# Kernel tuning notes

Hardware: AMD Instinct MI355X
Metric: run time of the kernel (lower is better)

Reference implementation:

```python
import jax, jax.numpy as jnp
import numpy as np

LN_EPS = 1e-5        # torch default LayerNorm eps
DEB_EPS = 1e-7       # deberta-v3 layer_norm_eps
ATT_SPAN = 256       # deberta-v3-base position_buckets -> pos_ebd_size
MAX_REL = 100        # config.max_relative_positions override


def _ln(x, g, b, eps):
    m = x.mean(-1, keepdims=True)
    v = jnp.var(x, axis=-1, keepdims=True)
    return (x - m) * jax.lax.rsqrt(v + eps) * g + b


def _lin(x, w, b):
    return x @ w.T + b


def _rel_buckets(L):
    # build_relative_position + make_log_bucket_position (bucket_size=256, max_position=100)
    rel = jnp.arange(L, dtype=jnp.int32)[:, None] - jnp.arange(L, dtype=jnp.int32)[None, :]
    mid = ATT_SPAN // 2
    sign = jnp.sign(rel)
    abs_pos = jnp.where((rel < mid) & (rel > -mid), mid - 1, jnp.abs(rel))
    log_pos = jnp.ceil(jnp.log(abs_pos.astype(jnp.float32) / mid)
                       / np.float32(np.log((MAX_REL - 1) / mid)) * (mid - 1)) + mid
    return jnp.where(abs_pos <= mid, rel, (log_pos * sign).astype(jnp.int32))


def _forward(ints, floats):
    type_ids, landmark_ids, mask = ints
    (xs, ys, zs, type_emb, landmark_emb, type_ln_g, type_ln_b, lm_ln_g, lm_ln_b,
     pos_w, pos_b, lt_in_w, lt_in_b, lt_out_w, lt_out_b, lt_ln1_g, lt_ln1_b,
     lt_ff1_w, lt_ff1_b, lt_ff2_w, lt_ff2_b, lt_ln2_g, lt_ln2_b,
     rel_emb, rel_ln_g, rel_ln_b, dq_w, dq_b, dk_w, dk_b, dv_w, dv_b,
     dao_w, dao_b, da_ln_g, da_ln_b, di_w, di_b, do_w, do_b, do_ln_g, do_ln_b,
     head_w, head_b) = floats

    # embeddings (padding_idx=0 -> zero row & zero grad) + layernorms + pos projection
    te = _ln(type_emb[type_ids] * (type_ids != 0)[..., None].astype(jnp.float32), type_ln_g, type_ln_b, LN_EPS)
    le = _ln(landmark_emb[landmark_ids] * (landmark_ids != 0)[..., None].astype(jnp.float32), lm_ln_g, lm_ln_b, LN_EPS)
    pe = _lin(jnp.stack([xs, ys, zs], -1), pos_w, pos_b)
    fts = jnp.concatenate([te, le, pe], -1)                  # [B,F,L,768]
    B, F, L, D = fts.shape
    h = fts.reshape(B * F, L, D)

    # --- nn.TransformerEncoderLayer over landmarks (post-norm, relu, nhead=1) ---
    q, k, v = jnp.split(_lin(h, lt_in_w, lt_in_b), 3, axis=-1)
    probs = jax.nn.softmax(jnp.einsum('bqd,bkd->bqk', q, k) / np.float32(np.sqrt(D)), axis=-1)
    attn = _lin(jnp.einsum('bqk,bkd->bqd', probs, v), lt_out_w, lt_out_b)
    h = _ln(h + attn, lt_ln1_g, lt_ln1_b, LN_EPS)
    ff = _lin(jax.nn.relu(_lin(h, lt_ff1_w, lt_ff1_b)), lt_ff2_w, lt_ff2_b)
    h = _ln(h + ff, lt_ln2_g, lt_ln2_b, LN_EPS)

    h = h.reshape(B, F, L, D).mean(2)                        # [B,F,768]

    # --- DebertaV2 layer over frames (disentangled attention, 1 head) ---
    m = mask[:, :, 0] > 0                                    # [B,F]
    q = _lin(h, dq_w, dq_b)
    k = _lin(h, dk_w, dk_b)
    v = _lin(h, dv_w, dv_b)
    scale = np.float32(np.sqrt(D * 3))                       # scale_factor = 1 + len({c2p,p2c})
    scores = jnp.einsum('bqd,bkd->bqk', q, k) / scale
    rel_ln = _ln(rel_emb, rel_ln_g, rel_ln_b, DEB_EPS)       # norm_rel_ebd='layer_norm'
    pos_q = _lin(rel_ln, dq_w, dq_b)                         # share_att_key=True
    pos_k = _lin(rel_ln, dk_w, dk_b)
    rel = _rel_buckets(F)                                    # [F,F]
    c2p_idx = jnp.clip(rel + ATT_SPAN, 0, 2 * ATT_SPAN - 1)
    c2p = jnp.einsum('bqd,rd->bqr', q, pos_k)                # [B,F,512]
    c2p = jnp.take_along_axis(c2p, jnp.broadcast_to(c2p_idx[None], (B, F, F)), axis=-1)
    p2c_idx = jnp.clip(-rel + ATT_SPAN, 0, 2 * ATT_SPAN - 1)
    p2c = jnp.einsum('bkd,rd->bkr', k, pos_q)                # [B,F,512]
    p2c = jnp.take_along_axis(p2c, jnp.broadcast_to(p2c_idx[None], (B, F, F)), axis=-1)
    scores = scores + (c2p + jnp.swapaxes(p2c, -1, -2)) / scale
    amask = m[:, :, None] & m[:, None, :]                    # XSoftmax mask
    probs = jax.nn.softmax(jnp.where(amask, scores, jnp.finfo(scores.dtype).min), axis=-1)
    probs = jnp.where(amask, probs, 0.0)
    ctx = jnp.einsum('bqk,bkd->bqd', probs, v)
    h = _ln(_lin(ctx, dao_w, dao_b) + h, da_ln_g, da_ln_b, DEB_EPS)
    inter = jax.nn.gelu(_lin(h, di_w, di_b), approximate=False)
    h = _ln(_lin(inter, do_w, do_b) + h, do_ln_g, do_ln_b, DEB_EPS)

    return _lin(h.mean(1), head_w, head_b)                   # [B,250]


def setup_inputs():
    ks = iter(jax.random.split(jax.random.key(0), 64))
    B, F, L, E, D, DF, NC = 8, 80, 100, 256, 768, 3072, 250
    def w(*shape):
        return jax.random.normal(next(ks), shape, dtype=jnp.float32) * 0.02
    z = lambda *s: jnp.zeros(s, jnp.float32)
    o = lambda *s: jnp.ones(s, jnp.float32)
    return {
        "type_ids": jax.random.randint(next(ks), (B, F, L), 0, 12, dtype=jnp.int32),
        "landmark_ids": jax.random.randint(next(ks), (B, F, L), 0, 127, dtype=jnp.int32),
        "xs": jax.random.normal(next(ks), (B, F, L), dtype=jnp.float32),
        "ys": jax.random.normal(next(ks), (B, F, L), dtype=jnp.float32),
        "zs": jax.random.normal(next(ks), (B, F, L), dtype=jnp.float32),
        "mask": jnp.ones((B, F, L), jnp.int32),
        "type_emb": w(12, E), "landmark_emb": w(127, E),
        "type_ln_g": o(E), "type_ln_b": z(E), "lm_ln_g": o(E), "lm_ln_b": z(E),
        "pos_w": w(E, 3), "pos_b": z(E),
        "lt_in_w": w(3 * D, D), "lt_in_b": z(3 * D), "lt_out_w": w(D, D), "lt_out_b": z(D),
        "lt_ln1_g": o(D), "lt_ln1_b": z(D),
        "lt_ff1_w": w(D, D), "lt_ff1_b": z(D), "lt_ff2_w": w(D, D), "lt_ff2_b": z(D),
        "lt_ln2_g": o(D), "lt_ln2_b": z(D),
        "rel_emb": w(2 * ATT_SPAN, D), "rel_ln_g": o(D), "rel_ln_b": z(D),
        "dq_w": w(D, D), "dq_b": z(D), "dk_w": w(D, D), "dk_b": z(D), "dv_w": w(D, D), "dv_b": z(D),
        "dao_w": w(D, D), "dao_b": z(D), "da_ln_g": o(D), "da_ln_b": z(D),
        "di_w": w(DF, D), "di_b": z(DF), "do_w": w(D, DF), "do_b": z(D),
        "do_ln_g": o(D), "do_ln_b": z(D),
        "head_w": w(NC, D), "head_b": z(NC),
    }


def reference(type_ids, landmark_ids, xs, ys, zs, mask, type_emb, landmark_emb,
              type_ln_g, type_ln_b, lm_ln_g, lm_ln_b, pos_w, pos_b,
              lt_in_w, lt_in_b, lt_out_w, lt_out_b, lt_ln1_g, lt_ln1_b,
              lt_ff1_w, lt_ff1_b, lt_ff2_w, lt_ff2_b, lt_ln2_g, lt_ln2_b,
              rel_emb, rel_ln_g, rel_ln_b, dq_w, dq_b, dk_w, dk_b, dv_w, dv_b,
              dao_w, dao_b, da_ln_g, da_ln_b, di_w, di_b, do_w, do_b,
              do_ln_g, do_ln_b, head_w, head_b):
    floats = (xs, ys, zs, type_emb, landmark_emb, type_ln_g, type_ln_b, lm_ln_g, lm_ln_b,
              pos_w, pos_b, lt_in_w, lt_in_b, lt_out_w, lt_out_b, lt_ln1_g, lt_ln1_b,
              lt_ff1_w, lt_ff1_b, lt_ff2_w, lt_ff2_b, lt_ln2_g, lt_ln2_b,
              rel_emb, rel_ln_g, rel_ln_b, dq_w, dq_b, dk_w, dk_b, dv_w, dv_b,
              dao_w, dao_b, da_ln_g, da_ln_b, di_w, di_b, do_w, do_b, do_ln_g, do_ln_b,
              head_w, head_b)
    return _forward((type_ids, landmark_ids, mask), floats)
```

## Files before the change

### kernel.cpp

```cpp
#include <hip/hip_runtime.h>

using short8v = __attribute__((ext_vector_type(8))) short;
using float4v = __attribute__((ext_vector_type(4))) float;

__device__ __forceinline__ unsigned short f2bf(float f) {
  unsigned int u = __float_as_uint(f);
  u += 0x7FFF + ((u >> 16) & 1);
  return (unsigned short)(u >> 16);
}
__device__ __forceinline__ float bf2f(unsigned short u) {
  return __uint_as_float((unsigned int)u << 16);
}

__device__ __forceinline__ int swz(int row, int c) {
  return row * 64 + (c ^ ((row & 7) << 3));
}

template<int BM, int ACT, bool OUTBF, int RES>
__global__ __launch_bounds__(256) void gemm_mfma(
    const unsigned short* __restrict__ A, const unsigned short* __restrict__ B,
    const float* __restrict__ bias, const void* __restrict__ resid, int ldr,
    void* __restrict__ Cv,
    int M, int N, int K, int lda, int ldb, int ldc,
    long long sA, long long sB, long long sC, long long sBias, float alpha)
{
  constexpr int NF = BM / 32;
  A += (long long)blockIdx.z * sA;
  B += (long long)blockIdx.z * sB;
  if (bias) bias += (long long)blockIdx.z * sBias;
  const int m0 = blockIdx.y * BM, n0 = blockIdx.x * BM;

  __shared__ __align__(16) unsigned short As[BM * 64];
  __shared__ __align__(16) unsigned short Bs[BM * 64];

  const int tid = threadIdx.x;
  const int w = tid >> 6, lane = tid & 63;
  const int wr = w >> 1, wc = w & 1;

  const int r0 = tid >> 3;
  const int c8 = (tid & 7) * 8;
  int ra[NF], rb[NF], soff[NF];
  #pragma unroll
  for (int i = 0; i < NF; ++i) {
    int r = m0 + r0 + i * 32; ra[i] = r < M - 1 ? r : M - 1;
    int q = n0 + r0 + i * 32; rb[i] = q < N - 1 ? q : N - 1;
    soff[i] = swz(r0 + i * 32, c8);
  }

  const int fr = lane & 15;
  const int fk = (lane >> 4) * 8;

  float4v acc[NF][NF] = {};

  short8v pa[NF], pb[NF];
  #pragma unroll
  for (int i = 0; i < NF; ++i) {
    pa[i] = *(const short8v*)(A + (long long)ra[i] * lda + c8);
    pb[i] = *(const short8v*)(B + (long long)rb[i] * ldb + c8);
  }

  for (int k0 = 0; k0 < K; k0 += 64) {
    __syncthreads();
    #pragma unroll
    for (int i = 0; i < NF; ++i) {
      *(short8v*)&As[soff[i]] = pa[i];
      *(short8v*)&Bs[soff[i]] = pb[i];
    }
    __syncthreads();
    if (k0 + 64 < K) {
      #pragma unroll
      for (int i = 0; i < NF; ++i) {
        pa[i] = *(const short8v*)(A + (long long)ra[i] * lda + k0 + 64 + c8);
        pb[i] = *(const short8v*)(B + (long long)rb[i] * ldb + k0 + 64 + c8);
      }
    }
    #pragma unroll
    for (int kk = 0; kk < 2; ++kk) {
      short8v a[NF], b[NF];
      #pragma unroll
      for (int i = 0; i < NF; ++i) {
        a[i] = *(const short8v*)&As[swz(wr * (NF * 16) + i * 16 + fr, kk * 32 + fk)];
        b[i] = *(const short8v*)&Bs[swz(wc * (NF * 16) + i * 16 + fr, kk * 32 + fk)];
      }
      #pragma unroll
      for (int mi = 0; mi < NF; ++mi)
        #pragma unroll
        for (int ni = 0; ni < NF; ++ni)
          acc[mi][ni] = __builtin_amdgcn_mfma_f32_16x16x32_bf16(a[mi], b[ni], acc[mi][ni], 0, 0, 0);
    }
  }

  const int ccol0 = n0 + wc * (NF * 16) + (lane & 15);
  const int crow0 = m0 + wr * (NF * 16) + (lane >> 4) * 4;
  float* Cf = (float*)Cv + (long long)blockIdx.z * sC;
  unsigned short* Cb = (unsigned short*)Cv + (long long)blockIdx.z * sC;
  #pragma unroll
  for (int ni = 0; ni < NF; ++ni) {
    const int col = ccol0 + ni * 16;
    if (col >= N) continue;
    const float bs = bias ? bias[col] : 0.f;
    #pragma unroll
    for (int mi = 0; mi < NF; ++mi) {
      #pragma unroll
      for (int r = 0; r < 4; ++r) {
        const int row = crow0 + mi * 16 + r;
        if (row >= M) continue;
        float v = acc[mi][ni][r] * alpha + bs;
        if (RES == 1) v += bf2f(((const unsigned short*)resid)[(long long)row * ldr + col]);
        if (RES == 2) v += ((const float*)resid)[(long long)row * ldr + col];
        if (ACT == 1) v = fmaxf(v, 0.f);
        if (ACT == 2) v = 0.5f * v * (1.f + erff(v * 0.70710678118654752f));
        if (OUTBF) Cb[(long long)row * ldc + col] = f2bf(v);
        else       Cf[(long long)row * ldc + col] = v;
      }
    }
  }
}

static void mg(hipStream_t st, int bm, int act, bool outbf, int res,
               const unsigned short* A, const unsigned short* B,
               const float* bias, const void* resid, int ldr, void* C,
               int M, int N, int K, int lda, int ldb, int ldc,
               long long sA, long long sB, long long sC, long long sBias,
               int bat, float alpha)
{
  dim3 grid((N + bm - 1) / bm, (M + bm - 1) / bm, bat);
  dim3 blk(256);
  #define GEMM_CALL(BM_, A_, O_, R_) \
    gemm_mfma<BM_, A_, O_, R_><<<grid, blk, 0, st>>>(A, B, bias, resid, ldr, C, \
        M, N, K, lda, ldb, ldc, sA, sB, sC, sBias, alpha)
  if (bm == 128) {
    if (outbf) {
      if (act == 1)       GEMM_CALL(128, 1, true, 0);
      else if (res == 1)  GEMM_CALL(128, 0, true, 1);
      else                GEMM_CALL(128, 0, true, 0);
    } else {
      GEMM_CALL(128, 0, false, 0);
    }
  } else {
    if (outbf) {
      if (act == 2)       GEMM_CALL(64, 2, true, 0);
      else                GEMM_CALL(64, 0, true, 0);
    } else {
      if (res == 2)       GEMM_CALL(64, 0, false, 2);
      else                GEMM_CALL(64, 0, false, 0);
    }
  }
  #undef GEMM_CALL
}

struct ConvArgs {
  const float* s[10];
  unsigned short* d[10];
  long long off[11];
};
__global__ __launch_bounds__(256) void convall_kernel(ConvArgs a, long long tot)
{
  const long long i = ((long long)blockIdx.x * 256 + threadIdx.x) * 4;
  if (i >= tot) return;
  int t = 0;
  while (i >= a.off[t + 1]) ++t;
  const long long j = i - a.off[t];
  const float4 v = *(const float4*)(a.s[t] + j);
  const unsigned int lo = (unsigned int)f2bf(v.x) | ((unsigned int)f2bf(v.y) << 16);
  const unsigned int hi = (unsigned int)f2bf(v.z) | ((unsigned int)f2bf(v.w) << 16);
  *(uint2*)(a.d[t] + j) = make_uint2(lo, hi);
}

__global__ __launch_bounds__(256) void embed_kernel(
    const int* __restrict__ tids, const int* __restrict__ lids,
    const float* __restrict__ xs, const float* __restrict__ ys, const float* __restrict__ zs,
    const float* __restrict__ temb, const float* __restrict__ lemb,
    const float* __restrict__ tg, const float* __restrict__ tb,
    const float* __restrict__ lg, const float* __restrict__ lb,
    const float* __restrict__ pw, const float* __restrict__ pb,
    unsigned short* __restrict__ hb)
{
  const int tok = blockIdx.x * 4 + (threadIdx.x >> 6);
  const int lane = threadIdx.x & 63;
  const int e0 = lane * 4;
  const int ti = tids[tok], li = lids[tok];
  float4 tv = make_float4(0.f, 0.f, 0.f, 0.f);
  float4 lv = make_float4(0.f, 0.f, 0.f, 0.f);
  if (ti != 0) tv = *(const float4*)(temb + ti * 256 + e0);
  if (li != 0) lv = *(const float4*)(lemb + li * 256 + e0);

  float s0 = tv.x + tv.y + tv.z + tv.w;
  float s1 = tv.x * tv.x + tv.y * tv.y + tv.z * tv.z + tv.w * tv.w;
  float s2 = lv.x + lv.y + lv.z + lv.w;
  float s3 = lv.x * lv.x + lv.y * lv.y + lv.z * lv.z + lv.w * lv.w;
  #pragma unroll
  for (int off = 32; off > 0; off >>= 1) {
    s0 += __shfl_xor(s0, off, 64);
    s1 += __shfl_xor(s1, off, 64);
    s2 += __shfl_xor(s2, off, 64);
    s3 += __shfl_xor(s3, off, 64);
  }
  const float mt = s0 * (1.f / 256.f), vt = s1 * (1.f / 256.f) - mt * mt;
  const float ml = s2 * (1.f / 256.f), vl = s3 * (1.f / 256.f) - ml * ml;
  const float rt = rsqrtf(vt + 1e-5f), rl = rsqrtf(vl + 1e-5f);

  const float4 tg4 = *(const float4*)(tg + e0), tb4 = *(const float4*)(tb + e0);
  const float4 lg4 = *(const float4*)(lg + e0), lb4 = *(const float4*)(lb + e0);
  const size_t base = (size_t)tok * 768;
  ushort4 o;
  o.x = f2bf((tv.x - mt) * rt * tg4.x + tb4.x);
  o.y = f2bf((tv.y - mt) * rt * tg4.y + tb4.y);
  o.z = f2bf((tv.z - mt) * rt * tg4.z + tb4.z);
  o.w = f2bf((tv.w - mt) * rt * tg4.w + tb4.w);
  *(ushort4*)(hb + base + e0) = o;
  o.x = f2bf((lv.x - ml) * rl * lg4.x + lb4.x);
  o.y = f2bf((lv.y - ml) * rl * lg4.y + lb4.y);
  o.z = f2bf((lv.z - ml) * rl * lg4.z + lb4.z);
  o.w = f2bf((lv.w - ml) * rl * lg4.w + lb4.w);
  *(ushort4*)(hb + base + 256 + e0) = o;

  const float X = xs[tok], Y = ys[tok], Z = zs[tok];
  const float4 w0 = *(const float4*)(pw + 12 * lane);
  const float4 w1 = *(const float4*)(pw + 12 * lane + 4);
  const float4 w2 = *(const float4*)(pw + 12 * lane + 8);
  const float4 pb4 = *(const float4*)(pb + e0);
  o.x = f2bf(w0.x * X + w0.y * Y + w0.z * Z + pb4.x);
  o.y = f2bf(w0.w * X + w1.x * Y + w1.y * Z + pb4.y);
  o.z = f2bf(w1.z * X + w1.w * Y + w2.x * Z + pb4.z);
  o.w = f2bf(w2.y * X + w2.z * Y + w2.w * Z + pb4.w);
  *(ushort4*)(hb + base + 512 + e0) = o;
}

template<int XBF, int RBF>
__global__ __launch_bounds__(256) void ln_kernel(
    const void* __restrict__ x, const void* __restrict__ res,
    const float* __restrict__ g, const float* __restrict__ b,
    float* __restrict__ yf, unsigned short* __restrict__ yb,
    int nrows, float eps)
{
  const int row = blockIdx.x * 4 + (threadIdx.x >> 6);
  if (row >= nrows) return;
  const int lane = threadIdx.x & 63;
  const size_t base = (size_t)row * 768;
  const int e0 = lane * 12;
  float v[12];
  #pragma unroll
  for (int j = 0; j < 3; ++j) {
    if (XBF) {
      const ushort4 u = *(const ushort4*)((const unsigned short*)x + base + e0 + 4 * j);
      v[4*j+0] = bf2f(u.x); v[4*j+1] = bf2f(u.y); v[4*j+2] = bf2f(u.z); v[4*j+3] = bf2f(u.w);
    } else {
      const float4 f = *(const float4*)((const float*)x + base + e0 + 4 * j);
      v[4*j+0] = f.x; v[4*j+1] = f.y; v[4*j+2] = f.z; v[4*j+3] = f.w;
    }
  }
  if (res) {
    #pragma unroll
    for (int j = 0; j < 3; ++j) {
      if (RBF) {
        const ushort4 u = *(const ushort4*)((const unsigned short*)res + base + e0 + 4 * j);
        v[4*j+0] += bf2f(u.x); v[4*j+1] += bf2f(u.y); v[4*j+2] += bf2f(u.z); v[4*j+3] += bf2f(u.w);
      } else {
        const float4 f = *(const float4*)((const float*)res + base + e0 + 4 * j);
        v[4*j+0] += f.x; v[4*j+1] += f.y; v[4*j+2] += f.z; v[4*j+3] += f.w;
      }
    }
  }
  float s = 0.f, ss = 0.f;
  #pragma unroll
  for (int j = 0; j < 12; ++j) { s += v[j]; ss += v[j] * v[j]; }
  #pragma unroll
  for (int off = 32; off > 0; off >>= 1) {
    s += __shfl_xor(s, off, 64);
    ss += __shfl_xor(ss, off, 64);
  }
  const float mean = s * (1.f / 768.f);
  const float rstd = rsqrtf(ss * (1.f / 768.f) - mean * mean + eps);
  #pragma unroll
  for (int j = 0; j < 3; ++j) {
    const float4 g4 = *(const float4*)(g + e0 + 4 * j);
    const float4 b4 = *(const float4*)(b + e0 + 4 * j);
    float o0 = (v[4*j+0] - mean) * rstd * g4.x + b4.x;
    float o1 = (v[4*j+1] - mean) * rstd * g4.y + b4.y;
    float o2 = (v[4*j+2] - mean) * rstd * g4.z + b4.z;
    float o3 = (v[4*j+3] - mean) * rstd * g4.w + b4.w;
    if (yf) *(float4*)(yf + base + e0 + 4 * j) = make_float4(o0, o1, o2, o3);
    if (yb) {
      ushort4 u; u.x = f2bf(o0); u.y = f2bf(o1); u.z = f2bf(o2); u.w = f2bf(o3);
      *(ushort4*)(yb + base + e0 + 4 * j) = u;
    }
  }
}

__global__ __launch_bounds__(256) void vtrans_kernel(
    const unsigned short* __restrict__ v, unsigned short* __restrict__ vt,
    int Lk, int rs, long long sIn, long long sOut)
{
  __shared__ unsigned short s[64][132];
  const int b = blockIdx.y, d0 = blockIdx.x * 64;
  const unsigned short* vb = v + (long long)b * sIn;
  unsigned short* ob = vt + (long long)b * sOut;
  for (int idx = threadIdx.x; idx < 128 * 64; idx += 256) {
    const int k = idx >> 6, dd = idx & 63;
    s[dd][k] = (k < Lk) ? vb[(long long)k * rs + d0 + dd] : (unsigned short)0;
  }
  __syncthreads();
  for (int idx = threadIdx.x; idx < 64 * 128; idx += 256) {
    const int dd = idx >> 7, k = idx & 127;
    ob[(long long)(d0 + dd) * 128 + k] = s[dd][k];
  }
}

__global__ __launch_bounds__(256) void sm2_kernel(
    const float* __restrict__ P32, unsigned short* __restrict__ Pbf, int nrows)
{
  const int rid = blockIdx.x * 4 + (threadIdx.x >> 6);
  if (rid >= nrows) return;
  const int z = rid / 100, q = rid - z * 100;
  const int lane = threadIdx.x & 63;
  const float* row = P32 + (size_t)z * 16384 + (size_t)q * 128;
  unsigned short* orow = Pbf + (size_t)z * 16384 + (size_t)q * 128;
  const float v0 = row[lane];
  const float v1 = (lane + 64 < 100) ? row[lane + 64] : -3.4e38f;
  float m = fmaxf(v0, v1);
  #pragma unroll
  for (int off = 32; off > 0; off >>= 1) m = fmaxf(m, __shfl_xor(m, off, 64));
  const float e0 = expf(v0 - m);
  const float e1 = (lane + 64 < 100) ? expf(v1 - m) : 0.f;
  float s = e0 + e1;
  #pragma unroll
  for (int off = 32; off > 0; off >>= 1) s += __shfl_xor(s, off, 64);
  const float inv = 1.f / s;
  orow[lane] = f2bf(e0 * inv);
  orow[lane + 64] = (lane + 64 < 100) ? f2bf(e1 * inv) : (unsigned short)0;
}

__global__ __launch_bounds__(256) void deb3_kernel(
    const float* __restrict__ sc,
    const float* __restrict__ c2p,
    const float* __restrict__ p2c,
    const int* __restrict__ mask,
    unsigned short* __restrict__ probs)
{
  const int rid = blockIdx.x * 4 + (threadIdx.x >> 6);
  if (rid >= 640) return;
  const int b = rid / 80, q = rid - b * 80;
  const int lane = threadIdx.x & 63;
  const bool mq = mask[(size_t)rid * 100] > 0;
  float v0 = -3.4e38f, v1 = -3.4e38f;
  bool val0 = false, val1 = false;
  {
    const int k = lane;
    const bool mk = mask[(size_t)(b * 80 + k) * 100] > 0;
    val0 = mq && mk;
    const int r = 256 + q - k;
    if (val0)
      v0 = sc[(size_t)b * 16384 + (size_t)q * 128 + k] +
           (c2p[(size_t)rid * 512 + r] + p2c[(size_t)(b * 80 + k) * 512 + r]) * (1.f / 48.f);
  }
  if (lane + 64 < 80) {
    const int k = lane + 64;
    const bool mk = mask[(size_t)(b * 80 + k) * 100] > 0;
    val1 = mq && mk;
    const int r = 256 + q - k;
    if (val1)
      v1 = sc[(size_t)b * 16384 + (size_t)q * 128 + k] +
           (c2p[(size_t)rid * 512 + r] + p2c[(size_t)(b * 80 + k) * 512 + r]) * (1.f / 48.f);
  }
  float m = fmaxf(v0, v1);
  #pragma unroll
  for (int off = 32; off > 0; off >>= 1) m = fmaxf(m, __shfl_xor(m, off, 64));
  const float e0 = val0 ? expf(v0 - m) : 0.f;
  const float e1 = val1 ? expf(v1 - m) : 0.f;
  float s = e0 + e1;
  #pragma unroll
  for (int off = 32; off > 0; off >>= 1) s += __shfl_xor(s, off, 64);
  const float inv = (s > 0.f) ? 1.f / s : 0.f;
  unsigned short* orow = probs + (size_t)b * 16384 + (size_t)q * 128;
  orow[lane] = val0 ? f2bf(e0 * inv) : (unsigned short)0;
  orow[lane + 64] = val1 ? f2bf(e1 * inv) : (unsigned short)0;
}

__global__ __launch_bounds__(192) void meanL_kernel(
    const unsigned short* __restrict__ hb, float* __restrict__ hf,
    unsigned short* __restrict__ hfb)
{
  const int bf = blockIdx.x;
  const int d0 = threadIdx.x * 4;
  float4 acc = make_float4(0.f, 0.f, 0.f, 0.f);
  for (int l = 0; l < 100; ++l) {
    const ushort4 u = *(const ushort4*)(hb + ((size_t)bf * 100 + l) * 768 + d0);
    acc.x += bf2f(u.x); acc.y += bf2f(u.y); acc.z += bf2f(u.z); acc.w += bf2f(u.w);
  }
  acc.x *= 0.01f; acc.y *= 0.01f; acc.z *= 0.01f; acc.w *= 0.01f;
  *(float4*)(hf + (size_t)bf * 768 + d0) = acc;
  ushort4 o; o.x = f2bf(acc.x); o.y = f2bf(acc.y); o.z = f2bf(acc.z); o.w = f2bf(acc.w);
  *(ushort4*)(hfb + (size_t)bf * 768 + d0) = o;
}

__global__ __launch_bounds__(192) void meanF_kernel(const float* __restrict__ h4, float* __restrict__ hm)
{
  const int b = blockIdx.x;
  const int d0 = threadIdx.x * 4;
  float4 acc = make_float4(0.f, 0.f, 0.f, 0.f);
  for (int f = 0; f < 80; ++f) {
    const float4 u = *(const float4*)(h4 + ((size_t)b * 80 + f) * 768 + d0);
    acc.x += u.x; acc.y += u.y; acc.z += u.z; acc.w += u.w;
  }
  const float k = 1.f / 80.f;
  *(float4*)(hm + (size_t)b * 768 + d0) = make_float4(acc.x * k, acc.y * k, acc.z * k, acc.w * k);
}

__global__ __launch_bounds__(64) void head_kernel(
    const float* __restrict__ hm, const float* __restrict__ w,
    const float* __restrict__ bias, float* __restrict__ out)
{
  const int n = blockIdx.x, b = blockIdx.y;
  const float* x = hm + (size_t)b * 768;
  const float* wn = w + (size_t)n * 768;
  float s = 0.f;
  for (int i = threadIdx.x * 4; i < 768; i += 256) {
    const float4 xv = *(const float4*)(x + i);
    const float4 wv = *(const float4*)(wn + i);
    s += xv.x * wv.x + xv.y * wv.y + xv.z * wv.z + xv.w * wv.w;
  }
  #pragma unroll
  for (int off = 32; off > 0; off >>= 1) s += __shfl_down(s, off, 64);
  if (threadIdx.x == 0) out[(size_t)b * 250 + n] = s + bias[n];
}

extern "C" void kernel_launch(void* const* d_in, const int* in_sizes, int n_in,
                              void* d_out, int out_size, void* d_ws, size_t ws_size,
                              hipStream_t stream)
{
  const int*   type_ids   = (const int*)  d_in[0];
  const int*   lm_ids     = (const int*)  d_in[1];
  const float* xs         = (const float*)d_in[2];
  const float* ys         = (const float*)d_in[3];
  const float* zs         = (const float*)d_in[4];
  const int*   mask       = (const int*)  d_in[5];
  const float* type_emb   = (const float*)d_in[6];
  const float* lm_emb     = (const float*)d_in[7];
  const float* type_ln_g  = (const float*)d_in[8];
  const float* type_ln_b  = (const float*)d_in[9];
  const float* lm_ln_g    = (const float*)d_in[10];
  const float* lm_ln_b    = (const float*)d_in[11];
  const float* pos_w      = (const float*)d_in[12];
  const float* pos_b      = (const float*)d_in[13];
  const float* lt_in_w    = (const float*)d_in[14];
  const float* lt_in_b    = (const float*)d_in[15];
  const float* lt_out_w   = (const float*)d_in[16];
  const float* lt_out_b   = (const float*)d_in[17];
  const float* lt_ln1_g   = (const float*)d_in[18];
  const float* lt_ln1_b   = (const float*)d_in[19];
  const float* lt_ff1_w   = (const float*)d_in[20];
  const float* lt_ff1_b   = (const float*)d_in[21];
  const float* lt_ff2_w   = (const float*)d_in[22];
  const float* lt_ff2_b   = (const float*)d_in[23];
  const float* lt_ln2_g   = (const float*)d_in[24];
  const float* lt_ln2_b   = (const float*)d_in[25];
  const float* rel_emb    = (const float*)d_in[26];
  const float* rel_ln_g   = (const float*)d_in[27];
  const float* rel_ln_b   = (const float*)d_in[28];
  const float* dq_w       = (const float*)d_in[29];
  const float* dq_b       = (const float*)d_in[30];
  const float* dk_w       = (const float*)d_in[31];
  const float* dk_b       = (const float*)d_in[32];
  const float* dv_w       = (const float*)d_in[33];
  const float* dv_b       = (const float*)d_in[34];
  const float* dao_w      = (const float*)d_in[35];
  const float* dao_b      = (const float*)d_in[36];
  const float* da_ln_g    = (const float*)d_in[37];
  const float* da_ln_b    = (const float*)d_in[38];
  const float* di_w       = (const float*)d_in[39];
  const float* di_b       = (const float*)d_in[40];
  const float* do_w       = (const float*)d_in[41];
  const float* do_b       = (const float*)d_in[42];
  const float* do_ln_g    = (const float*)d_in[43];
  const float* do_ln_b    = (const float*)d_in[44];
  const float* head_w     = (const float*)d_in[45];
  const float* head_b     = (const float*)d_in[46];
  float* out = (float*)d_out;
  float* ws  = (float*)d_ws;

  const float inv_sqrt_d = 0.03608439182435161f;
  const long long W2 = 768 * 768;

  auto rnd = [](size_t x) { return (x + 63) & ~(size_t)63; };
  const size_t ws_floats = ws_size / sizeof(float);

  size_t o = 0;
  const size_t offHB = o; o += rnd((size_t)64000 * 768 / 2);
  auto woff = [&](size_t elems) { size_t r = o; o += rnd(elems / 2); return r; };
  const size_t w_in   = woff((size_t)2304 * 768);
  const size_t w_out  = woff((size_t)768 * 768);
  const size_t w_f1   = woff((size_t)768 * 768);
  const size_t w_f2   = woff((size_t)768 * 768);
  const size_t w_qkv3 = woff((size_t)2304 * 768);
  const size_t w_ao   = woff((size_t)768 * 768);
  const size_t w_di   = woff((size_t)3072 * 768);
  const size_t w_do   = woff((size_t)768 * 3072);
  const size_t b_qkv3 = o; o += rnd(2304);
  const size_t scratch0 = o;

  size_t s3need = 0;
  {
    size_t t = 0;
    t += rnd((size_t)640 * 768);
    t += rnd((size_t)640 * 768 / 2);
    t += rnd((size_t)640 * 2304 / 2);
    t += rnd((size_t)512 * 768 / 2);
    t += rnd((size_t)512 * 1536 / 2);
    t += 2 * (size_t)640 * 512;
    t += rnd((size_t)8 * 16384);
    t += rnd((size_t)8 * 16384 / 2);
    t += rnd((size_t)8 * 98304 / 2);
    t += rnd((size_t)640 * 768 / 2);
    t += 2 * rnd((size_t)640 * 768);
    t += rnd((size_t)640 * 768 / 2);
    t += rnd((size_t)640 * 3072 / 2);
    t += 2 * rnd((size_t)640 * 768);
    t += rnd((size_t)8 * 768);
    s3need = t;
  }

  auto chunk_need = [&](int c) {
    const size_t R = (size_t)c * 100;
    size_t t = 0;
    t += rnd(R * 2304 / 2);
    t += 4 * rnd(R * 768 / 2);
    t += rnd((size_t)c * 98304 / 2);
    t += rnd((size_t)c * 16384);
    t += rnd((size_t)c * 16384 / 2);
    return t;
  };
  int C = 1;
  {
    const int cands[] = {640, 320, 160, 80, 40, 20, 10, 5, 2, 1};
    for (int c : cands) {
      const size_t need = scratch0 + (chunk_need(c) > s3need ? chunk_need(c) : s3need);
      if (need <= ws_floats) { C = c; break; }
    }
  }
  const size_t R = (size_t)C * 100;

  o = scratch0;
  const size_t qkvb = o; o += rnd(R * 2304 / 2);
  const size_t ctxb = o; o += rnd(R * 768 / 2);
  const size_t t1b  = o; o += rnd(R * 768 / 2);
  const size_t h1bb = o; o += rnd(R * 768 / 2);
  const size_t ffob = o; o += rnd(R * 768 / 2);
  const size_t vtb  = o; o += rnd((size_t)C * 98304 / 2);
  const size_t p32  = o; o += rnd((size_t)C * 16384);
  const size_t pbf  = o; o += rnd((size_t)C * 16384 / 2);

  auto US = [&](size_t foff) { return (unsigned short*)(ws + foff); };

  {
    ConvArgs a;
    const float* srcs[10] = {lt_in_w, lt_out_w, lt_ff1_w, lt_ff2_w,
                             dq_w, dk_w, dv_w, dao_w, di_w, do_w};
    unsigned short* dsts[10] = {US(w_in), US(w_out), US(w_f1), US(w_f2),
                                US(w_qkv3), US(w_qkv3) + W2, US(w_qkv3) + 2 * W2,
                                US(w_ao), US(w_di), US(w_do)};
    const long long ns[10] = {2304 * 768, W2, W2, W2, W2, W2, W2, W2,
                              3072 * 768, 3072 * 768};
    long long tot = 0;
    for (int i = 0; i < 10; ++i) { a.s[i] = srcs[i]; a.d[i] = dsts[i]; a.off[i] = tot; tot += ns[i]; }
    a.off[10] = tot;
    convall_kernel<<<(unsigned)((tot / 4 + 255) / 256), 256, 0, stream>>>(a, tot);
  }
  hipMemcpyAsync(ws + b_qkv3,        dq_b, 768 * sizeof(float), hipMemcpyDeviceToDevice, stream);
  hipMemcpyAsync(ws + b_qkv3 + 768,  dk_b, 768 * sizeof(float), hipMemcpyDeviceToDevice, stream);
  hipMemcpyAsync(ws + b_qkv3 + 1536, dv_b, 768 * sizeof(float), hipMemcpyDeviceToDevice, stream);

  embed_kernel<<<16000, 256, 0, stream>>>(type_ids, lm_ids, xs, ys, zs,
      type_emb, lm_emb, type_ln_g, type_ln_b, lm_ln_g, lm_ln_b, pos_w, pos_b,
      US(offHB));

  for (int c0 = 0; c0 < 640; c0 += C) {
    unsigned short* hbc = US(offHB) + (size_t)c0 * 100 * 768;
    const int Rr = C * 100;
    mg(stream, 128, 0, true, 0, hbc, US(w_in), lt_in_b, nullptr, 0, US(qkvb),
       Rr, 2304, 768, 768, 768, 2304, 0, 0, 0, 0, 1, 1.f);
    mg(stream, 128, 0, false, 0, US(qkvb), US(qkvb) + 768, nullptr, nullptr, 0, ws + p32,
       100, 100, 768, 2304, 2304, 128, 230400, 230400, 16384, 0, C, inv_sqrt_d);
    sm2_kernel<<<(Rr + 3) / 4, 256, 0, stream>>>(ws + p32, US(pbf), Rr);
    vtrans_kernel<<<dim3(12, C), 256, 0, stream>>>(US(qkvb) + 1536, US(vtb), 100, 2304, 230400, 98304);
    mg(stream, 128, 0, true, 0, US(pbf), US(vtb), nullptr, nullptr, 0, US(ctxb),
       100, 768, 128, 128, 128, 768, 16384, 98304, 76800, 0, C, 1.f);
    mg(stream, 128, 0, true, 1, US(ctxb), US(w_out), lt_out_b, hbc, 768, US(t1b),
       Rr, 768, 768, 768, 768, 768, 0, 0, 0, 0, 1, 1.f);
    ln_kernel<1, 1><<<(Rr + 3) / 4, 256, 0, stream>>>(US(t1b), nullptr,
        lt_ln1_g, lt_ln1_b, nullptr, US(h1bb), Rr, 1e-5f);
    mg(stream, 128, 1, true, 0, US(h1bb), US(w_f1), lt_ff1_b, nullptr, 0, US(ffob),
       Rr, 768, 768, 768, 768, 768, 0, 0, 0, 0, 1, 1.f);
    mg(stream, 128, 0, true, 1, US(ffob), US(w_f2), lt_ff2_b, US(h1bb), 768, US(t1b),
       Rr, 768, 768, 768, 768, 768, 0, 0, 0, 0, 1, 1.f);
    ln_kernel<1, 1><<<(Rr + 3) / 4, 256, 0, stream>>>(US(t1b), nullptr,
        lt_ln2_g, lt_ln2_b, nullptr, hbc, Rr, 1e-5f);
  }

  o = scratch0;
  const size_t hf    = o; o += rnd((size_t)640 * 768);
  const size_t hfb   = o; o += rnd((size_t)640 * 768 / 2);
  const size_t qkv3b = o; o += rnd((size_t)640 * 2304 / 2);
  const size_t rlnb  = o; o += rnd((size_t)512 * 768 / 2);
  const size_t posb  = o; o += rnd((size_t)512 * 1536 / 2);
  const size_t c2p   = o; o += (size_t)640 * 512;
  const size_t p2c   = o; o += (size_t)640 * 512;
  const size_t p32_3 = o; o += rnd((size_t)8 * 16384);
  const size_t p3bf  = o; o += rnd((size_t)8 * 16384 / 2);
  const size_t vt3b  = o; o += rnd((size_t)8 * 98304 / 2);
  const size_t ctx3b = o; o += rnd((size_t)640 * 768 / 2);
  const size_t t3    = o; o += rnd((size_t)640 * 768);
  const size_t h3    = o; o += rnd((size_t)640 * 768);
  const size_t h3b   = o; o += rnd((size_t)640 * 768 / 2);
  const size_t interb= o; o += rnd((size_t)640 * 3072 / 2);
  const size_t t4    = o; o += rnd((size_t)640 * 768);
  const size_t h4    = o; o += rnd((size_t)640 * 768);
  const size_t hm    = o; o += rnd((size_t)8 * 768);

  meanL_kernel<<<640, 192, 0, stream>>>(US(offHB), ws + hf, US(hfb));
  mg(stream, 64, 0, true, 0, US(hfb), US(w_qkv3), ws + b_qkv3, nullptr, 0, US(qkv3b),
     640, 2304, 768, 768, 768, 2304, 0, 0, 0, 0, 1, 1.f);
  ln_kernel<0, 0><<<128, 256, 0, stream>>>(rel_emb, nullptr,
      rel_ln_g, rel_ln_b, nullptr, US(rlnb), 512, 1e-7f);
  mg(stream, 64, 0, true, 0, US(rlnb), US(w_qkv3) + W2, ws + b_qkv3 + 768, nullptr, 0, US(posb),
     512, 768, 768, 768, 768, 1536, 0, -W2, 768, -768, 2, 1.f);
  mg(stream, 64, 0, false, 0, US(qkv3b), US(qkv3b) + 768, nullptr, nullptr, 0, ws + p32_3,
     80, 80, 768, 2304, 2304, 128, 184320, 184320, 16384, 0, 8, 1.f / 48.f);
  mg(stream, 64, 0, false, 0, US(qkv3b), US(posb), nullptr, nullptr, 0, ws + c2p,
     640, 512, 768, 2304, 1536, 512, 768, 768, 327680, 0, 2, 1.f);
  deb3_kernel<<<160, 256, 0, stream>>>(ws + p32_3, ws + c2p, ws + p2c, mask, US(p3bf));
  vtrans_kernel<<<dim3(12, 8), 256, 0, stream>>>(US(qkv3b) + 1536, US(vt3b), 80, 2304, 184320, 98304);
  mg(stream, 64, 0, true, 0, US(p3bf), US(vt3b), nullptr, nullptr, 0, US(ctx3b),
     80, 768, 128, 128, 128, 768, 16384, 98304, 61440, 0, 8, 1.f);
  mg(stream, 64, 0, false, 2, US(ctx3b), US(w_ao), dao_b, ws + hf, 768, ws + t3,
     640, 768, 768, 768, 768, 768, 0, 0, 0, 0, 1, 1.f);
  ln_kernel<0, 0><<<160, 256, 0, stream>>>(ws + t3, nullptr,
      da_ln_g, da_ln_b, ws + h3, US(h3b), 640, 1e-7f);
  mg(stream, 64, 2, true, 0, US(h3b), US(w_di), di_b, nullptr, 0, US(interb),
     640, 3072, 768, 768, 768, 3072, 0, 0, 0, 0, 1, 1.f);
  mg(stream, 64, 0, false, 2, US(interb), US(w_do), do_b, ws + h3, 768, ws + t4,
     640, 768, 3072, 3072, 3072, 768, 0, 0, 0, 0, 1, 1.f);
  ln_kernel<0, 0><<<160, 256, 0, stream>>>(ws + t4, nullptr,
      do_ln_g, do_ln_b, ws + h4, nullptr, 640, 1e-7f);
  meanF_kernel<<<8, 192, 0, stream>>>(ws + h4, ws + hm);
  head_kernel<<<dim3(250, 8), 64, 0, stream>>>(ws + hm, head_w, head_b, out);
}
```

Baseline: 1.923 ms.

## Fuse QK scores, softmax and PV into one attention kernel; merge QKV/pos GEMMs

Adds an attn_fused kernel that computes QK^T with MFMA, applies the scale, masking and relative-position bias (c2p/p2c) plus softmax in registers, and then multiplies by V^T from LDS, all in one block per batch. It replaces the separate score GEMM, softmax kernel and PV GEMM in both the landmark transformer and the DeBERTa layer, which removes fp32 score round trips and several launches. It also stacks the rel-embedding LN output beneath the hidden states so one 1152-row GEMM produces QKV and position projections together, with the c2p/p2c GEMM reading from that buffer. The trade-off is that each fused launch has only one block per batch (grid 1x1xC), so parallelism is low and each block does the whole PV sweep serially.

```diff
diff --git a/kernel.cpp b/kernel.cpp
--- a/kernel.cpp
+++ b/kernel.cpp
@@ -147,6 +147,227 @@
     }
   }
   #undef GEMM_CALL
+}
+
+template<int MODE>
+__global__ __launch_bounds__(256) void attn_fused(
+    const unsigned short* __restrict__ Q, const unsigned short* __restrict__ Kp,
+    const unsigned short* __restrict__ VT,
+    const float* __restrict__ c2p, const float* __restrict__ p2c,
+    const int* __restrict__ mask,
+    unsigned short* __restrict__ O,
+    int Mv, int K, int lda, int ldvt, int ldc,
+    long long sQ, long long sVT, long long sO, float alpha)
+{
+  const int z = blockIdx.z;
+  Q  += (long long)z * sQ;
+  Kp += (long long)z * sQ;
+  VT += (long long)z * sVT;
+  O  += (long long)z * sO;
+
+  __shared__ __align__(16) unsigned short As[128 * 64];
+  __shared__ __align__(16) unsigned short Bs[128 * 64];
+  __shared__ __align__(16) unsigned short Pl[128 * 128];
+  float* ovl = (float*)As;
+  int*   smk = (int*)(ovl + 512);
+
+  const int tid = threadIdx.x;
+  const int w = tid >> 6, lane = tid & 63;
+  const int wr = w >> 1, wc = w & 1;
+  const int r0 = tid >> 3, c8 = (tid & 7) * 8;
+
+  int ra[4], soff[4];
+  #pragma unroll
+  for (int i = 0; i < 4; ++i) {
+    int r = r0 + i * 32;
+    ra[i] = (r < Mv - 1 ? r : Mv - 1);
+    soff[i] = swz(r, c8);
+  }
+  const int fr = lane & 15, fk = (lane >> 4) * 8;
+
+  float4v acc[4][4] = {};
+  short8v pa[4], pb[4];
+  #pragma unroll
+  for (int i = 0; i < 4; ++i) {
+    pa[i] = *(const short8v*)(Q  + (long long)ra[i] * lda + c8);
+    pb[i] = *(const short8v*)(Kp + (long long)ra[i] * lda + c8);
+  }
+  for (int k0 = 0; k0 < K; k0 += 64) {
+    __syncthreads();
+    #pragma unroll
+    for (int i = 0; i < 4; ++i) {
+      *(short8v*)&As[soff[i]] = pa[i];
+      *(short8v*)&Bs[soff[i]] = pb[i];
+    }
+    __syncthreads();
+    if (k0 + 64 < K) {
+      #pragma unroll
+      for (int i = 0; i < 4; ++i) {
+        pa[i] = *(const short8v*)(Q  + (long long)ra[i] * lda + k0 + 64 + c8);
+        pb[i] = *(const short8v*)(Kp + (long long)ra[i] * lda + k0 + 64 + c8);
+      }
+    }
+    #pragma unroll
+    for (int kk = 0; kk < 2; ++kk) {
+      short8v a[4], b[4];
+      #pragma unroll
+      for (int i = 0; i < 4; ++i) {
+        a[i] = *(const short8v*)&As[swz(wr * 64 + i * 16 + fr, kk * 32 + fk)];
+        b[i] = *(const short8v*)&Bs[swz(wc * 64 + i * 16 + fr, kk * 32 + fk)];
+      }
+      #pragma unroll
+      for (int mi = 0; mi < 4; ++mi)
+        #pragma unroll
+        for (int ni = 0; ni < 4; ++ni)
+          acc[mi][ni] = __builtin_amdgcn_mfma_f32_16x16x32_bf16(a[mi], b[ni], acc[mi][ni], 0, 0, 0);
+    }
+  }
+
+  __syncthreads();
+  if (MODE == 3 && tid < 80) smk[tid] = mask[((long long)z * 80 + tid) * 100];
+  __syncthreads();
+
+  const int g = lane >> 4, f = lane & 15;
+  const int colB = wc * 64 + f;
+  const int rowB = wr * 64 + g * 4;
+
+  bool cv[4];
+  #pragma unroll
+  for (int ni = 0; ni < 4; ++ni) {
+    const int col = colB + ni * 16;
+    cv[ni] = (MODE == 2) ? (col < Mv) : (col < 80 && smk[col] != 0);
+  }
+
+  float lm[4][4];
+  #pragma unroll
+  for (int mi = 0; mi < 4; ++mi) {
+    #pragma unroll
+    for (int r = 0; r < 4; ++r) {
+      const int row = rowB + mi * 16 + r;
+      const bool rv = (MODE == 2) ? true : (row < 80 && smk[row] != 0);
+      float mx = -3.4e38f;
+      #pragma unroll
+      for (int ni = 0; ni < 4; ++ni) {
+        float v = acc[mi][ni][r] * alpha;
+        const int col = colB + ni * 16;
+        const bool valid = rv && cv[ni];
+        if (MODE == 3 && valid) {
+          const int rr = 256 + row - col;
+          v += (c2p[((long long)z * 80 + row) * 512 + rr] +
+                p2c[((long long)z * 80 + col) * 512 + rr]) * alpha;
+        }
+        v = valid ? v : -3.4e38f;
+        acc[mi][ni][r] = v;
+        mx = fmaxf(mx, v);
+      }
+      #pragma unroll
+      for (int off = 1; off < 16; off <<= 1) mx = fmaxf(mx, __shfl_xor(mx, off, 64));
+      lm[mi][r] = mx;
+    }
+  }
+  if (f == 0) {
+    #pragma unroll
+    for (int mi = 0; mi < 4; ++mi)
+      #pragma unroll
+      for (int r = 0; r < 4; ++r)
+        ovl[wc * 128 + rowB + mi * 16 + r] = lm[mi][r];
+  }
+  __syncthreads();
+  float ls[4][4], mfin[4][4];
+  #pragma unroll
+  for (int mi = 0; mi < 4; ++mi) {
+    #pragma unroll
+    for (int r = 0; r < 4; ++r) {
+      const int row = rowB + mi * 16 + r;
+      const float m = fmaxf(lm[mi][r], ovl[(wc ^ 1) * 128 + row]);
+      mfin[mi][r] = m;
+      float s = 0.f;
+      #pragma unroll
+      for (int ni = 0; ni < 4; ++ni) {
+        const float v = acc[mi][ni][r];
+        const float e = (v > -1e37f) ? expf(v - m) : 0.f;
+        acc[mi][ni][r] = e;
+        s += e;
+      }
+      #pragma unroll
+      for (int off = 1; off < 16; off <<= 1) s += __shfl_xor(s, off, 64);
+      ls[mi][r] = s;
+    }
+  }
+  if (f == 0) {
+    #pragma unroll
+    for (int mi = 0; mi < 4; ++mi)
+      #pragma unroll
+      for (int r = 0; r < 4; ++r)
+        ovl[256 + wc * 128 + rowB + mi * 16 + r] = ls[mi][r];
+  }
+  __syncthreads();
+  #pragma unroll
+  for (int mi = 0; mi < 4; ++mi) {
+    #pragma unroll
+    for (int r = 0; r < 4; ++r) {
+      const int row = rowB + mi * 16 + r;
+      const float tot = ls[mi][r] + ovl[256 + (wc ^ 1) * 128 + row];
+      const float inv = (tot > 0.f) ? 1.f / tot : 0.f;
+      #pragma unroll
+      for (int ni = 0; ni < 4; ++ni) {
+        const int col = colB + ni * 16;
+        Pl[row * 128 + (col ^ ((row & 7) << 3))] = f2bf(acc[mi][ni][r] * inv);
+      }
+    }
+  }
+  __syncthreads();
+
+  for (int n0 = 0; n0 < 768; n0 += 128) {
+    short8v v0[4], v1[4];
+    #pragma unroll
+    for (int i = 0; i < 4; ++i) {
+      const int rv = n0 + r0 + i * 32;
+      v0[i] = *(const short8v*)(VT + (long long)rv * ldvt + c8);
+      v1[i] = *(const short8v*)(VT + (long long)rv * ldvt + 64 + c8);
+    }
+    __syncthreads();
+    #pragma unroll
+    for (int i = 0; i < 4; ++i) {
+      *(short8v*)&As[soff[i]] = v0[i];
+      *(short8v*)&Bs[soff[i]] = v1[i];
+    }
+    __syncthreads();
+
+    float4v oacc[4][4] = {};
+    #pragma unroll
+    for (int half = 0; half < 2; ++half) {
+      const unsigned short* src = half ? Bs : As;
+      #pragma unroll
+      for (int kk = 0; kk < 2; ++kk) {
+        const int kglob = half * 64 + kk * 32 + fk;
+        short8v a[4], b[4];
+        #pragma unroll
+        for (int i = 0; i < 4; ++i) {
+          const int prow = wr * 64 + i * 16 + fr;
+          a[i] = *(const short8v*)&Pl[prow * 128 + (kglob ^ ((prow & 7) << 3))];
+          b[i] = *(const short8v*)&src[swz(wc * 64 + i * 16 + fr, kk * 32 + fk)];
+        }
+        #pragma unroll
+        for (int mi = 0; mi < 4; ++mi)
+          #pragma unroll
+          for (int ni = 0; ni < 4; ++ni)
+            oacc[mi][ni] = __builtin_amdgcn_mfma_f32_16x16x32_bf16(a[mi], b[ni], oacc[mi][ni], 0, 0, 0);
+      }
+    }
+    #pragma unroll
+    for (int ni = 0; ni < 4; ++ni) {
+      const int col = n0 + colB + ni * 16;
+      #pragma unroll
+      for (int mi = 0; mi < 4; ++mi) {
+        #pragma unroll
+        for (int r = 0; r < 4; ++r) {
+          const int row = rowB + mi * 16 + r;
+          if (row < Mv) O[(long long)row * ldc + col] = f2bf(oacc[mi][ni][r]);
+        }
+      }
+    }
+  }
 }
 
 struct ConvArgs {
@@ -246,8 +467,8 @@
       const ushort4 u = *(const ushort4*)((const unsigned short*)x + base + e0 + 4 * j);
       v[4*j+0] = bf2f(u.x); v[4*j+1] = bf2f(u.y); v[4*j+2] = bf2f(u.z); v[4*j+3] = bf2f(u.w);
     } else {
-      const float4 f = *(const float4*)((const float*)x + base + e0 + 4 * j);
-      v[4*j+0] = f.x; v[4*j+1] = f.y; v[4*j+2] = f.z; v[4*j+3] = f.w;
+      const float4 fx = *(const float4*)((const float*)x + base + e0 + 4 * j);
+      v[4*j+0] = fx.x; v[4*j+1] = fx.y; v[4*j+2] = fx.z; v[4*j+3] = fx.w;
     }
   }
   if (res) {
@@ -257,8 +478,8 @@
         const ushort4 u = *(const ushort4*)((const unsigned short*)res + base + e0 + 4 * j);
         v[4*j+0] += bf2f(u.x); v[4*j+1] += bf2f(u.y); v[4*j+2] += bf2f(u.z); v[4*j+3] += bf2f(u.w);
       } else {
-        const float4 f = *(const float4*)((const float*)res + base + e0 + 4 * j);
-        v[4*j+0] += f.x; v[4*j+1] += f.y; v[4*j+2] += f.z; v[4*j+3] += f.w;
+        const float4 fx = *(const float4*)((const float*)res + base + e0 + 4 * j);
+        v[4*j+0] += fx.x; v[4*j+1] += fx.y; v[4*j+2] += fx.z; v[4*j+3] += fx.w;
       }
     }
   }
@@ -305,76 +526,6 @@
     const int dd = idx >> 7, k = idx & 127;
     ob[(long long)(d0 + dd) * 128 + k] = s[dd][k];
   }
-}
-
-__global__ __launch_bounds__(256) void sm2_kernel(
-    const float* __restrict__ P32, unsigned short* __restrict__ Pbf, int nrows)
-{
-  const int rid = blockIdx.x * 4 + (threadIdx.x >> 6);
-  if (rid >= nrows) return;
-  const int z = rid / 100, q = rid - z * 100;
-  const int lane = threadIdx.x & 63;
-  const float* row = P32 + (size_t)z * 16384 + (size_t)q * 128;
-  unsigned short* orow = Pbf + (size_t)z * 16384 + (size_t)q * 128;
-  const float v0 = row[lane];
-  const float v1 = (lane + 64 < 100) ? row[lane + 64] : -3.4e38f;
-  float m = fmaxf(v0, v1);
-  #pragma unroll
-  for (int off = 32; off > 0; off >>= 1) m = fmaxf(m, __shfl_xor(m, off, 64));
-  const float e0 = expf(v0 - m);
-  const float e1 = (lane + 64 < 100) ? expf(v1 - m) : 0.f;
-  float s = e0 + e1;
-  #pragma unroll
-  for (int off = 32; off > 0; off >>= 1) s += __shfl_xor(s, off, 64);
-  const float inv = 1.f / s;
-  orow[lane] = f2bf(e0 * inv);
-  orow[lane + 64] = (lane + 64 < 100) ? f2bf(e1 * inv) : (unsigned short)0;
-}
-
-__global__ __launch_bounds__(256) void deb3_kernel(
-    const float* __restrict__ sc,
-    const float* __restrict__ c2p,
-    const float* __restrict__ p2c,
-    const int* __restrict__ mask,
-    unsigned short* __restrict__ probs)
-{
-  const int rid = blockIdx.x * 4 + (threadIdx.x >> 6);
-  if (rid >= 640) return;
-  const int b = rid / 80, q = rid - b * 80;
-  const int lane = threadIdx.x & 63;
-  const bool mq = mask[(size_t)rid * 100] > 0;
-  float v0 = -3.4e38f, v1 = -3.4e38f;
-  bool val0 = false, val1 = false;
-  {
-    const int k = lane;
-    const bool mk = mask[(size_t)(b * 80 + k) * 100] > 0;
-    val0 = mq && mk;
-    const int r = 256 + q - k;
-    if (val0)
-      v0 = sc[(size_t)b * 16384 + (size_t)q * 128 + k] +
-           (c2p[(size_t)rid * 512 + r] + p2c[(size_t)(b * 80 + k) * 512 + r]) * (1.f / 48.f);
-  }
-  if (lane + 64 < 80) {
-    const int k = lane + 64;
-    const bool mk = mask[(size_t)(b * 80 + k) * 100] > 0;
-    val1 = mq && mk;
-    const int r = 256 + q - k;
-    if (val1)
-      v1 = sc[(size_t)b * 16384 + (size_t)q * 128 + k] +
-           (c2p[(size_t)rid * 512 + r] + p2c[(size_t)(b * 80 + k) * 512 + r]) * (1.f / 48.f);
-  }
-  float m = fmaxf(v0, v1);
-  #pragma unroll
-  for (int off = 32; off > 0; off >>= 1) m = fmaxf(m, __shfl_xor(m, off, 64));
-  const float e0 = val0 ? expf(v0 - m) : 0.f;
-  const float e1 = val1 ? expf(v1 - m) : 0.f;
-  float s = e0 + e1;
-  #pragma unroll
-  for (int off = 32; off > 0; off >>= 1) s += __shfl_xor(s, off, 64);
-  const float inv = (s > 0.f) ? 1.f / s : 0.f;
-  unsigned short* orow = probs + (size_t)b * 16384 + (size_t)q * 128;
-  orow[lane] = val0 ? f2bf(e0 * inv) : (unsigned short)0;
-  orow[lane + 64] = val1 ? f2bf(e1 * inv) : (unsigned short)0;
 }
 
 __global__ __launch_bounds__(192) void meanL_kernel(
@@ -503,13 +654,9 @@
   {
     size_t t = 0;
     t += rnd((size_t)640 * 768);
-    t += rnd((size_t)640 * 768 / 2);
-    t += rnd((size_t)640 * 2304 / 2);
-    t += rnd((size_t)512 * 768 / 2);
-    t += rnd((size_t)512 * 1536 / 2);
+    t += rnd((size_t)1152 * 768 / 2);
+    t += rnd((size_t)1152 * 2304 / 2);
     t += 2 * (size_t)640 * 512;
-    t += rnd((size_t)8 * 16384);
-    t += rnd((size_t)8 * 16384 / 2);
     t += rnd((size_t)8 * 98304 / 2);
     t += rnd((size_t)640 * 768 / 2);
     t += 2 * rnd((size_t)640 * 768);
@@ -526,8 +673,6 @@
     t += rnd(R * 2304 / 2);
     t += 4 * rnd(R * 768 / 2);
     t += rnd((size_t)c * 98304 / 2);
-    t += rnd((size_t)c * 16384);
-    t += rnd((size_t)c * 16384 / 2);
     return t;
   };
   int C = 1;
@@ -547,8 +692,6 @@
   const size_t h1bb = o; o += rnd(R * 768 / 2);
   const size_t ffob = o; o += rnd(R * 768 / 2);
   const size_t vtb  = o; o += rnd((size_t)C * 98304 / 2);
-  const size_t p32  = o; o += rnd((size_t)C * 16384);
-  const size_t pbf  = o; o += rnd((size_t)C * 16384 / 2);
 
   auto US = [&](size_t foff) { return (unsigned short*)(ws + foff); };
 
@@ -579,12 +722,10 @@
     const int Rr = C * 100;
     mg(stream, 128, 0, true, 0, hbc, US(w_in), lt_in_b, nullptr, 0, US(qkvb),
        Rr, 2304, 768, 768, 768, 2304, 0, 0, 0, 0, 1, 1.f);
-    mg(stream, 128, 0, false, 0, US(qkvb), US(qkvb) + 768, nullptr, nullptr, 0, ws + p32,
-       100, 100, 768, 2304, 2304, 128, 230400, 230400, 16384, 0, C, inv_sqrt_d);
-    sm2_kernel<<<(Rr + 3) / 4, 256, 0, stream>>>(ws + p32, US(pbf), Rr);
     vtrans_kernel<<<dim3(12, C), 256, 0, stream>>>(US(qkvb) + 1536, US(vtb), 100, 2304, 230400, 98304);
-    mg(stream, 128, 0, true, 0, US(pbf), US(vtb), nullptr, nullptr, 0, US(ctxb),
-       100, 768, 128, 128, 128, 768, 16384, 98304, 76800, 0, C, 1.f);
+    attn_fused<2><<<dim3(1, 1, C), 256, 0, stream>>>(
+        US(qkvb), US(qkvb) + 768, US(vtb), nullptr, nullptr, nullptr, US(ctxb),
+        100, 768, 2304, 128, 768, 230400, 98304, 76800, inv_sqrt_d);
     mg(stream, 128, 0, true, 1, US(ctxb), US(w_out), lt_out_b, hbc, 768, US(t1b),
        Rr, 768, 768, 768, 768, 768, 0, 0, 0, 0, 1, 1.f);
     ln_kernel<1, 1><<<(Rr + 3) / 4, 256, 0, stream>>>(US(t1b), nullptr,
@@ -599,14 +740,10 @@
 
   o = scratch0;
   const size_t hf    = o; o += rnd((size_t)640 * 768);
-  const size_t hfb   = o; o += rnd((size_t)640 * 768 / 2);
-  const size_t qkv3b = o; o += rnd((size_t)640 * 2304 / 2);
-  const size_t rlnb  = o; o += rnd((size_t)512 * 768 / 2);
-  const size_t posb  = o; o += rnd((size_t)512 * 1536 / 2);
+  const size_t hfbE  = o; o += rnd((size_t)1152 * 768 / 2);
+  const size_t qp    = o; o += rnd((size_t)1152 * 2304 / 2);
   const size_t c2p   = o; o += (size_t)640 * 512;
   const size_t p2c   = o; o += (size_t)640 * 512;
-  const size_t p32_3 = o; o += rnd((size_t)8 * 16384);
-  const size_t p3bf  = o; o += rnd((size_t)8 * 16384 / 2);
   const size_t vt3b  = o; o += rnd((size_t)8 * 98304 / 2);
   const size_t ctx3b = o; o += rnd((size_t)640 * 768 / 2);
   const size_t t3    = o; o += rnd((size_t)640 * 768);
@@ -617,21 +754,17 @@
   const size_t h4    = o; o += rnd((size_t)640 * 768);
   const size_t hm    = o; o += rnd((size_t)8 * 768);
 
-  meanL_kernel<<<640, 192, 0, stream>>>(US(offHB), ws + hf, US(hfb));
-  mg(stream, 64, 0, true, 0, US(hfb), US(w_qkv3), ws + b_qkv3, nullptr, 0, US(qkv3b),
-     640, 2304, 768, 768, 768, 2304, 0, 0, 0, 0, 1, 1.f);
+  meanL_kernel<<<640, 192, 0, stream>>>(US(offHB), ws + hf, US(hfbE));
   ln_kernel<0, 0><<<128, 256, 0, stream>>>(rel_emb, nullptr,
-      rel_ln_g, rel_ln_b, nullptr, US(rlnb), 512, 1e-7f);
-  mg(stream, 64, 0, true, 0, US(rlnb), US(w_qkv3) + W2, ws + b_qkv3 + 768, nullptr, 0, US(posb),
-     512, 768, 768, 768, 768, 1536, 0, -W2, 768, -768, 2, 1.f);
-  mg(stream, 64, 0, false, 0, US(qkv3b), US(qkv3b) + 768, nullptr, nullptr, 0, ws + p32_3,
-     80, 80, 768, 2304, 2304, 128, 184320, 184320, 16384, 0, 8, 1.f / 48.f);
-  mg(stream, 64, 0, false, 0, US(qkv3b), US(posb), nullptr, nullptr, 0, ws + c2p,
-     640, 512, 768, 2304, 1536, 512, 768, 768, 327680, 0, 2, 1.f);
-  deb3_kernel<<<160, 256, 0, stream>>>(ws + p32_3, ws + c2p, ws + p2c, mask, US(p3bf));
-  vtrans_kernel<<<dim3(12, 8), 256, 0, stream>>>(US(qkv3b) + 1536, US(vt3b), 80, 2304, 184320, 98304);
-  mg(stream, 64, 0, true, 0, US(p3bf), US(vt3b), nullptr, nullptr, 0, US(ctx3b),
-     80, 768, 128, 128, 128, 768, 16384, 98304, 61440, 0, 8, 1.f);
+      rel_ln_g, rel_ln_b, nullptr, US(hfbE) + (size_t)640 * 768, 512, 1e-7f);
+  mg(stream, 64, 0, true, 0, US(hfbE), US(w_qkv3), ws + b_qkv3, nullptr, 0, US(qp),
+     1152, 2304, 768, 768, 768, 2304, 0, 0, 0, 0, 1, 1.f);
+  mg(stream, 64, 0, false, 0, US(qp), US(qp) + (size_t)640 * 2304 + 768, nullptr, nullptr, 0, ws + c2p,
+     640, 512, 768, 2304, 2304, 512, 768, -768, 327680, 0, 2, 1.f);
+  vtrans_kernel<<<dim3(12, 8), 256, 0, stream>>>(US(qp) + 1536, US(vt3b), 80, 2304, 184320, 98304);
+  attn_fused<3><<<dim3(1, 1, 8), 256, 0, stream>>>(
+      US(qp), US(qp) + 768, US(vt3b), ws + c2p, ws + p2c, mask, US(ctx3b),
+      80, 768, 2304, 128, 768, 184320, 98304, 61440, 1.f / 48.f);
   mg(stream, 64, 0, false, 2, US(ctx3b), US(w_ao), dao_b, ws + hf, 768, ws + t3,
      640, 768, 768, 768, 768, 768, 0, 0, 0, 0, 1, 1.f);
   ln_kernel<0, 0><<<160, 256, 0, stream>>>(ws + t3, nullptr,
```

Measured after the change: 2.171 ms. 12.9% more time.
